# Kernel tuning notes

Measured on AMD Instinct MI355X. Metric: run time of the kernel, lower is better.

Reference implementation:

```python
import jax, jax.numpy as jnp
import numpy as np

S, B, H, N = 512, 32, 512, 131072  # seq_len, batch, hidden_dim, num candidate spans
MAX_STEP = 20  # max_length


def setup_inputs() -> dict:
    key = jax.random.key(0)
    ks = jax.random.split(key, 8)
    hidden = jax.random.normal(ks[0], (S, B, 2 * H), dtype=jnp.float32)
    span_bids = jax.random.randint(ks[1], (N,), 0, B, dtype=jnp.int32)
    # begin in [1, S-1-MAX_STEP-1] so that begin-1>=0 and end=begin+step <= S-1
    span_begins = jax.random.randint(ks[2], (N,), 1, S - MAX_STEP - 2, dtype=jnp.int32)
    steps = jax.random.randint(ks[3], (N,), 2, MAX_STEP + 1, dtype=jnp.int32)
    span_ends = span_begins + steps
    span_flags = jax.random.randint(ks[4], (N,), 0, 2, dtype=jnp.int32)
    span_weights = jax.random.uniform(ks[5], (N,), dtype=jnp.float32)
    W1 = jax.random.normal(ks[6], (2 * H, H), dtype=jnp.float32) / np.sqrt(2.0 * H)
    b1 = jnp.zeros((H,), dtype=jnp.float32)
    W2 = jax.random.normal(ks[7], (H, 1), dtype=jnp.float32) / np.sqrt(float(H))
    b2 = jnp.zeros((1,), dtype=jnp.float32)
    return {"hidden": hidden, "span_bids": span_bids, "span_begins": span_begins,
            "span_ends": span_ends, "span_flags": span_flags, "span_weights": span_weights,
            "W1": W1, "b1": b1, "W2": W2, "b2": b2}


def reference(hidden, span_bids, span_begins, span_ends, span_flags, span_weights, W1, b1, W2, b2):
    h = W2.shape[0]  # hidden_dim
    # vectorized _span_embed: fwd diff on first half, bwd diff on second half
    fwd = hidden[span_ends - 1, span_bids, :h] - hidden[span_begins - 1, span_bids, :h]
    bwd = hidden[span_begins, span_bids, h:] - hidden[span_ends, span_bids, h:]
    feats = jnp.concatenate([fwd, bwd], axis=-1)  # [N, 2H]
    z = jnp.maximum(feats @ W1 + b1, 0.0)
    p = jax.nn.sigmoid(z @ W2 + b2)[:, 0]  # [N]
    targets = (span_flags == 1).astype(p.dtype)
    n_pos = jnp.sum(targets)
    n_tot = jnp.asarray(targets.shape[0], p.dtype)
    scale = 2.0 * n_pos / n_tot  # negative weights scaled by 2*P/(P+N)
    w_eff = jnp.where(span_flags == 1, span_weights, span_weights * scale)
    pc = jnp.clip(p, 1e-7, 1.0 - 1e-7)
    bce = -(targets * jnp.log(pc) + (1.0 - targets) * jnp.log(1.0 - pc))
    loss = jnp.mean(w_eff * bce)
    return loss
```

## Files before the change

kernel.cpp:

```cpp
#include <hip/hip_runtime.h>
#include <hip/hip_bf16.h>


typedef float f32x4 __attribute__((ext_vector_type(4)));
typedef float f32x2 __attribute__((ext_vector_type(2)));
typedef __bf16 bf16x8 __attribute__((ext_vector_type(8)));

__device__ __forceinline__ unsigned short f2bf(float f) {
  unsigned int u = __float_as_uint(f);
  u += 0x7fffu + ((u >> 16) & 1u);
  return (unsigned short)(u >> 16);
}
__device__ __forceinline__ float bf2f(unsigned int lo16) {
  return __uint_as_float(lo16 << 16);
}

__global__ void w1_blocked(const float* __restrict__ W1,
                           unsigned short* __restrict__ W1b) {
  int idx = blockIdx.x * 256 + threadIdx.x;
  int kc = idx & 3;
  int n  = (idx >> 2) & 511;
  int c  = idx >> 11;
  int k0 = c * 32 + kc * 8;
  unsigned short tmp[8];
#pragma unroll
  for (int j = 0; j < 8; ++j)
    tmp[j] = f2bf(W1[(k0 + j) * 512 + n]);
  *(uint4*)(W1b + c * 16384 + n * 32 + kc * 8) = *(uint4*)tmp;
}

#define APITCH 520
__global__ __launch_bounds__(256, 2) void proj_gemm(
    const float* __restrict__ hidden,
    const unsigned short* __restrict__ w1b,
    unsigned char* __restrict__ Wq) {
  __shared__ __align__(16) unsigned short AH[64 * APITCH];
  unsigned short* Eb = AH;

  const int t = threadIdx.x;
  const int lane = t & 63;
  const int w = t >> 6;
  const int r0 = blockIdx.x << 6;
  const int hk = blockIdx.y << 9;
  const int q = lane >> 4;
  const int m = lane & 15;

  {
    const int col = (t & 31) << 4;
    const int rsub = t >> 5;
#pragma unroll
    for (int p = 0; p < 8; ++p) {
      int row = (p << 3) + rsub;
      const float4* gp = (const float4*)(hidden + ((r0 + row) << 10) + hk + col);
      float4 f0 = gp[0], f1 = gp[1], f2 = gp[2], f3 = gp[3];
      uint4 a, b;
      a.x = (unsigned)f2bf(f0.x) | ((unsigned)f2bf(f0.y) << 16);
      a.y = (unsigned)f2bf(f0.z) | ((unsigned)f2bf(f0.w) << 16);
      a.z = (unsigned)f2bf(f1.x) | ((unsigned)f2bf(f1.y) << 16);
      a.w = (unsigned)f2bf(f1.z) | ((unsigned)f2bf(f1.w) << 16);
      b.x = (unsigned)f2bf(f2.x) | ((unsigned)f2bf(f2.y) << 16);
      b.y = (unsigned)f2bf(f2.z) | ((unsigned)f2bf(f2.w) << 16);
      b.z = (unsigned)f2bf(f3.x) | ((unsigned)f2bf(f3.y) << 16);
      b.w = (unsigned)f2bf(f3.z) | ((unsigned)f2bf(f3.w) << 16);
      unsigned short* dst = AH + row * APITCH + col;
      *(uint4*)dst = a;
      *(uint4*)(dst + 8) = b;
    }
  }
  __syncthreads();

  int boffn[8];
#pragma unroll
  for (int nt = 0; nt < 8; ++nt)
    boffn[nt] = (((w << 7) + (nt << 4) + m) << 5) + (q << 3);
  const unsigned short* w1base = w1b + (blockIdx.y << 18);

  f32x4 acc[4][8];
#pragma unroll
  for (int i = 0; i < 4; ++i)
#pragma unroll
    for (int j = 0; j < 8; ++j) acc[i][j] = (f32x4){0.f, 0.f, 0.f, 0.f};

#pragma unroll
  for (int it = 0; it < 16; ++it) {
    const unsigned short* bt = w1base + (it << 14);
    bf16x8 bfr[8];
#pragma unroll
    for (int nt = 0; nt < 8; ++nt)
      bfr[nt] = *(const bf16x8*)(bt + boffn[nt]);
    bf16x8 af[4];
#pragma unroll
    for (int mt = 0; mt < 4; ++mt)
      af[mt] = *(const bf16x8*)(AH + ((mt << 4) + m) * APITCH + (it << 5) + (q << 3));
#pragma unroll
    for (int mt = 0; mt < 4; ++mt)
#pragma unroll
      for (int nt = 0; nt < 8; ++nt)
        acc[mt][nt] = __builtin_amdgcn_mfma_f32_16x16x32_bf16(af[mt], bfr[nt],
                                                              acc[mt][nt], 0, 0, 0);
  }
  __syncthreads();

#pragma unroll
  for (int pass = 0; pass < 2; ++pass) {
#pragma unroll
    for (int mh = 0; mh < 2; ++mh) {
      int mt = (pass << 1) + mh;
#pragma unroll
      for (int r = 0; r < 4; ++r) {
        int rr = (mh << 4) + ((lane >> 4) << 2) + r;
#pragma unroll
        for (int nt = 0; nt < 8; ++nt)
          Eb[((w << 5) + rr) * 136 + (nt << 4) + (lane & 15)] = f2bf(acc[mt][nt][r]);
      }
    }
#pragma unroll
    for (int i = 0; i < 8; ++i) {
      int task = (i << 6) + lane;
      int rr = task >> 4;
      int ck = task & 15;
      uint4 v = *(const uint4*)&Eb[((w << 5) + rr) * 136 + (ck << 3)];
      float f0 = bf2f(v.x & 0xffff), f1 = bf2f(v.x >> 16);
      float f2 = bf2f(v.y & 0xffff), f3 = bf2f(v.y >> 16);
      float f4 = bf2f(v.z & 0xffff), f5 = bf2f(v.z >> 16);
      float f6 = bf2f(v.w & 0xffff), f7 = bf2f(v.w >> 16);
      uint2 o;
      o.x = __builtin_amdgcn_cvt_pk_fp8_f32(f0, f1, 0, false);
      o.x = __builtin_amdgcn_cvt_pk_fp8_f32(f2, f3, o.x, true);
      o.y = __builtin_amdgcn_cvt_pk_fp8_f32(f4, f5, 0, false);
      o.y = __builtin_amdgcn_cvt_pk_fp8_f32(f6, f7, o.y, true);
      int grow = r0 + (pass << 5) + rr;
      int col = (w << 7) + (ck << 3);
      if (hk == 0) {
        *(uint2*)(Wq + (grow << 10) + col) = o;
      } else if (grow >= 32) {
        *(uint2*)(Wq + ((grow - 32) << 10) + 512 + col) = o;
      }
    }
  }
}

#define SPB 64
__global__ __launch_bounds__(256) void span_eval(
    const unsigned char* __restrict__ Wq,
    const int* __restrict__ bids, const int* __restrict__ begins,
    const int* __restrict__ ends, const int* __restrict__ flags,
    const float* __restrict__ weights,
    const float* __restrict__ b1, const float* __restrict__ w2,
    const float* __restrict__ b2, float* __restrict__ partials) {
  __shared__ int oB[SPB], oE[SPB], sfl[SPB];
  __shared__ float swt[SPB];
  __shared__ float red[4][3];
  const int t = threadIdx.x;
  const int lane = t & 63;
  const int w = t >> 6;
  const int h = lane >> 5;
  const int hl = lane & 31;
  const int sbase = blockIdx.x * SPB;

  if (t < SPB) {
    int s = sbase + t;
    int b = bids[s], bg = begins[s], en = ends[s];
    oB[t] = (((bg - 1) << 5) + b) << 10;
    oE[t] = (((en - 1) << 5) + b) << 10;
    sfl[t] = flags[s];
    swt[t] = weights[s];
  }
  __syncthreads();

  const int sp0 = ((w << 1) + h) << 3;
  const int c0 = hl << 4;
  float b1v[16], w2v[16];
#pragma unroll
  for (int q = 0; q < 4; ++q) {
    float4 bv = *(const float4*)(b1 + c0 + (q << 2));
    float4 wv = *(const float4*)(w2 + c0 + (q << 2));
    b1v[(q << 2) + 0] = bv.x; b1v[(q << 2) + 1] = bv.y;
    b1v[(q << 2) + 2] = bv.z; b1v[(q << 2) + 3] = bv.w;
    w2v[(q << 2) + 0] = wv.x; w2v[(q << 2) + 1] = wv.y;
    w2v[(q << 2) + 2] = wv.z; w2v[(q << 2) + 3] = wv.w;
  }

  auto dec = [](unsigned int v, float* f) {
    f32x2 a = __builtin_amdgcn_cvt_pk_f32_fp8(v, false);
    f32x2 b = __builtin_amdgcn_cvt_pk_f32_fp8(v, true);
    f[0] = a[0]; f[1] = a[1]; f[2] = b[0]; f[3] = b[1];
  };

  uint4 BU[3], BV[3], EU[3], EV[3];
  auto ld = [&](int slot, int j) {
    int ob = oB[sp0 + j], oe = oE[sp0 + j];
    BU[slot] = *(const uint4*)(Wq + ob + c0);
    BV[slot] = *(const uint4*)(Wq + ob + 512 + c0);
    EU[slot] = *(const uint4*)(Wq + oe + c0);
    EV[slot] = *(const uint4*)(Wq + oe + 512 + c0);
  };
  ld(0, 0); ld(1, 1); ld(2, 2);

  float mylogit = 0.f;
#pragma unroll
  for (int j = 0; j < 8; ++j) {
    const int slot = j % 3;
    float buf[16], bvf[16], euf[16], evf[16];
    dec(BU[slot].x, buf); dec(BU[slot].y, buf + 4);
    dec(BU[slot].z, buf + 8); dec(BU[slot].w, buf + 12);
    dec(BV[slot].x, bvf); dec(BV[slot].y, bvf + 4);
    dec(BV[slot].z, bvf + 8); dec(BV[slot].w, bvf + 12);
    dec(EU[slot].x, euf); dec(EU[slot].y, euf + 4);
    dec(EU[slot].z, euf + 8); dec(EU[slot].w, euf + 12);
    dec(EV[slot].x, evf); dec(EV[slot].y, evf + 4);
    dec(EV[slot].z, evf + 8); dec(EV[slot].w, evf + 12);
    if (j + 3 < 8) ld(slot, j + 3);
    float sv = 0.f;
#pragma unroll
    for (int k = 0; k < 16; ++k) {
      float zp = euf[k] - buf[k] + bvf[k] - evf[k] + b1v[k];
      sv += fmaxf(zp, 0.f) * w2v[k];
    }
    sv += __shfl_xor(sv, 1);
    sv += __shfl_xor(sv, 2);
    sv += __shfl_xor(sv, 4);
    sv += __shfl_xor(sv, 8);
    sv += __shfl_xor(sv, 16);
    if (hl == j) mylogit = sv;
  }

  mylogit = __shfl(mylogit, ((lane & 8) << 2) + (lane & 7));

  float pos_t = 0.f, neg_t = 0.f, cnt_t = 0.f;
  if (lane < 16) {
    int sl = (w << 4) + lane;
    float logit = mylogit + b2[0];
    float p = 1.f / (1.f + expf(-logit));
    p = fminf(fmaxf(p, 1e-7f), 1.f - 1e-7f);
    int fl = sfl[sl];
    float bce = (fl == 1) ? -logf(p) : -logf(1.f - p);
    float term = swt[sl] * bce;
    pos_t = (fl == 1) ? term : 0.f;
    neg_t = (fl == 1) ? 0.f : term;
    cnt_t = (fl == 1) ? 1.f : 0.f;
  }
#pragma unroll
  for (int off = 1; off < 64; off <<= 1) {
    pos_t += __shfl_xor(pos_t, off);
    neg_t += __shfl_xor(neg_t, off);
    cnt_t += __shfl_xor(cnt_t, off);
  }
  if (lane == 0) { red[w][0] = pos_t; red[w][1] = neg_t; red[w][2] = cnt_t; }
  __syncthreads();
  if (t == 0) {
    partials[(blockIdx.x << 2) + 0] = red[0][0] + red[1][0] + red[2][0] + red[3][0];
    partials[(blockIdx.x << 2) + 1] = red[0][1] + red[1][1] + red[2][1] + red[3][1];
    partials[(blockIdx.x << 2) + 2] = red[0][2] + red[1][2] + red[2][2] + red[3][2];
  }
}

__global__ void finalize(const float* __restrict__ parts, int nblk,
                         float* __restrict__ out, int nspans) {
  __shared__ float sp[4], sn[4], sc[4];
  float P = 0.f, Ng = 0.f, C = 0.f;
  for (int i = threadIdx.x; i < nblk; i += 256) {
    P += parts[(i << 2) + 0];
    Ng += parts[(i << 2) + 1];
    C += parts[(i << 2) + 2];
  }
#pragma unroll
  for (int off = 1; off < 64; off <<= 1) {
    P += __shfl_xor(P, off);
    Ng += __shfl_xor(Ng, off);
    C += __shfl_xor(C, off);
  }
  int w = threadIdx.x >> 6;
  if ((threadIdx.x & 63) == 0) { sp[w] = P; sn[w] = Ng; sc[w] = C; }
  __syncthreads();
  if (threadIdx.x == 0) {
    P = sp[0] + sp[1] + sp[2] + sp[3];
    Ng = sn[0] + sn[1] + sn[2] + sn[3];
    C = sc[0] + sc[1] + sc[2] + sc[3];
    float scale = 2.f * C / (float)nspans;
    out[0] = (P + scale * Ng) / (float)nspans;
  }
}

extern "C" void kernel_launch(void* const* d_in, const int* in_sizes, int n_in,
                              void* d_out, int out_size, void* d_ws, size_t ws_size,
                              hipStream_t stream) {
  const float* hidden = (const float*)d_in[0];
  const int* bids     = (const int*)d_in[1];
  const int* begins   = (const int*)d_in[2];
  const int* ends     = (const int*)d_in[3];
  const int* flags    = (const int*)d_in[4];
  const float* weights = (const float*)d_in[5];
  const float* W1 = (const float*)d_in[6];
  const float* b1 = (const float*)d_in[7];
  const float* W2 = (const float*)d_in[8];
  const float* b2 = (const float*)d_in[9];
  float* out = (float*)d_out;
  const int nspans = in_sizes[1];
  const int nblk = nspans / SPB;

  float* partials = (float*)d_ws;
  unsigned short* W1b = (unsigned short*)((char*)d_ws + (1 << 18));
  unsigned char* Wq = (unsigned char*)((char*)d_ws + (2 << 20));

  w1_blocked<<<256, 256, 0, stream>>>(W1, W1b);
  proj_gemm<<<dim3(256, 2), 256, 0, stream>>>(hidden, W1b, Wq);
  span_eval<<<nblk, 256, 0, stream>>>(Wq, bids, begins, ends, flags, weights,
                                      b1, W2, b2, partials);
  finalize<<<1, 256, 0, stream>>>(partials, nblk, out, nspans);
}
```

Baseline: 174.9 us.

## Bucket spans by batch index and swizzle span_eval blocks for cache locality

Adds a histogram and scatter pass that counting-sorts span indices by batch id. span_eval then reads spans through this permutation, and its block indices are swizzled across 8 groups so that blocks running together touch the same batch's rows of the projected Wq table, which should improve L2 and MALL reuse of the gathered rows. The bf16 conversion in proj_gemm is also switched to native __bf16 casts. The cost is two extra small kernels, a memset, and indirect index loads.

```diff
diff --git a/kernel.cpp b/kernel.cpp
--- a/kernel.cpp
+++ b/kernel.cpp
@@ -29,6 +29,56 @@
   *(uint4*)(W1b + c * 16384 + n * 32 + kc * 8) = *(uint4*)tmp;
 }
 
+__global__ void span_hist(const int* __restrict__ bids, int* __restrict__ ghist,
+                          int nspans) {
+  __shared__ int h[32];
+  int t = threadIdx.x;
+  if (t < 32) h[t] = 0;
+  __syncthreads();
+  int base = blockIdx.x * 1024;
+#pragma unroll
+  for (int i = 0; i < 4; ++i) {
+    int idx = base + t + i * 256;
+    if (idx < nspans) atomicAdd(&h[bids[idx]], 1);
+  }
+  __syncthreads();
+  if (t < 32) atomicAdd(&ghist[t], h[t]);
+}
+
+__global__ void span_scatter(const int* __restrict__ bids,
+                             const int* __restrict__ ghist,
+                             int* __restrict__ gslot,
+                             int* __restrict__ sidx, int nspans) {
+  __shared__ int lh[32], lbase[32], lcur[32];
+  int t = threadIdx.x;
+  if (t < 32) lh[t] = 0;
+  __syncthreads();
+  int base = blockIdx.x * 512;
+  int myb[2];
+#pragma unroll
+  for (int i = 0; i < 2; ++i) {
+    int idx = base + t + i * 256;
+    myb[i] = (idx < nspans) ? bids[idx] : -1;
+    if (myb[i] >= 0) atomicAdd(&lh[myb[i]], 1);
+  }
+  __syncthreads();
+  if (t < 32) {
+    int pre = 0;
+    for (int j = 0; j < t; ++j) pre += ghist[j];
+    lbase[t] = pre + atomicAdd(&gslot[t], lh[t]);
+    lcur[t] = 0;
+  }
+  __syncthreads();
+#pragma unroll
+  for (int i = 0; i < 2; ++i) {
+    int b = myb[i];
+    if (b >= 0) {
+      int pos = lbase[b] + atomicAdd(&lcur[b], 1);
+      sidx[pos] = base + t + i * 256;
+    }
+  }
+}
+
 #define APITCH 520
 __global__ __launch_bounds__(256, 2) void proj_gemm(
     const float* __restrict__ hidden,
@@ -53,18 +103,18 @@
       int row = (p << 3) + rsub;
       const float4* gp = (const float4*)(hidden + ((r0 + row) << 10) + hk + col);
       float4 f0 = gp[0], f1 = gp[1], f2 = gp[2], f3 = gp[3];
-      uint4 a, b;
-      a.x = (unsigned)f2bf(f0.x) | ((unsigned)f2bf(f0.y) << 16);
-      a.y = (unsigned)f2bf(f0.z) | ((unsigned)f2bf(f0.w) << 16);
-      a.z = (unsigned)f2bf(f1.x) | ((unsigned)f2bf(f1.y) << 16);
-      a.w = (unsigned)f2bf(f1.z) | ((unsigned)f2bf(f1.w) << 16);
-      b.x = (unsigned)f2bf(f2.x) | ((unsigned)f2bf(f2.y) << 16);
-      b.y = (unsigned)f2bf(f2.z) | ((unsigned)f2bf(f2.w) << 16);
-      b.z = (unsigned)f2bf(f3.x) | ((unsigned)f2bf(f3.y) << 16);
-      b.w = (unsigned)f2bf(f3.z) | ((unsigned)f2bf(f3.w) << 16);
+      bf16x8 va, vb;
+      va[0] = (__bf16)f0.x; va[1] = (__bf16)f0.y;
+      va[2] = (__bf16)f0.z; va[3] = (__bf16)f0.w;
+      va[4] = (__bf16)f1.x; va[5] = (__bf16)f1.y;
+      va[6] = (__bf16)f1.z; va[7] = (__bf16)f1.w;
+      vb[0] = (__bf16)f2.x; vb[1] = (__bf16)f2.y;
+      vb[2] = (__bf16)f2.z; vb[3] = (__bf16)f2.w;
+      vb[4] = (__bf16)f3.x; vb[5] = (__bf16)f3.y;
+      vb[6] = (__bf16)f3.z; vb[7] = (__bf16)f3.w;
       unsigned short* dst = AH + row * APITCH + col;
-      *(uint4*)dst = a;
-      *(uint4*)(dst + 8) = b;
+      *(bf16x8*)dst = va;
+      *(bf16x8*)(dst + 8) = vb;
     }
   }
   __syncthreads();
@@ -143,6 +193,7 @@
 #define SPB 64
 __global__ __launch_bounds__(256) void span_eval(
     const unsigned char* __restrict__ Wq,
+    const int* __restrict__ sidx,
     const int* __restrict__ bids, const int* __restrict__ begins,
     const int* __restrict__ ends, const int* __restrict__ flags,
     const float* __restrict__ weights,
@@ -156,10 +207,17 @@
   const int w = t >> 6;
   const int h = lane >> 5;
   const int hl = lane & 31;
-  const int sbase = blockIdx.x * SPB;
+
+  const int nblk = gridDim.x;
+  int lb = blockIdx.x;
+  if ((nblk & 7) == 0) {
+    const int cpx = nblk >> 3;
+    lb = (blockIdx.x & 7) * cpx + (blockIdx.x >> 3);
+  }
+  const int sbase = lb * SPB;
 
   if (t < SPB) {
-    int s = sbase + t;
+    int s = sidx[sbase + t];
     int b = bids[s], bg = begins[s], en = ends[s];
     oB[t] = (((bg - 1) << 5) + b) << 10;
     oE[t] = (((en - 1) << 5) + b) << 10;
@@ -302,10 +360,17 @@
   float* partials = (float*)d_ws;
   unsigned short* W1b = (unsigned short*)((char*)d_ws + (1 << 18));
   unsigned char* Wq = (unsigned char*)((char*)d_ws + (2 << 20));
-
+  int* ghist = (int*)((char*)d_ws + (19 << 20));
+  int* gslot = ghist + 32;
+  int* sidx  = (int*)((char*)d_ws + (20 << 20));
+
+  hipMemsetAsync(ghist, 0, 64 * sizeof(int), stream);
   w1_blocked<<<256, 256, 0, stream>>>(W1, W1b);
+  span_hist<<<(nspans + 1023) / 1024, 256, 0, stream>>>(bids, ghist, nspans);
+  span_scatter<<<(nspans + 511) / 512, 256, 0, stream>>>(bids, ghist, gslot,
+                                                         sidx, nspans);
   proj_gemm<<<dim3(256, 2), 256, 0, stream>>>(hidden, W1b, Wq);
-  span_eval<<<nblk, 256, 0, stream>>>(Wq, bids, begins, ends, flags, weights,
-                                      b1, W2, b2, partials);
+  span_eval<<<nblk, 256, 0, stream>>>(Wq, sidx, bids, begins, ends, flags,
+                                      weights, b1, W2, b2, partials);
   finalize<<<1, 256, 0, stream>>>(partials, nblk, out, nspans);
 }
```

Measured after the change: 175.0 us. No clear change (+0.1%).
